# Kernel optimization log

Hardware: AMD Instinct MI355X
Metric: run time of the kernel (lower is better)

Reference implementation:

```python
import jax, jax.numpy as jnp
import numpy as np

N_USERS = 100000
N_ITEMS = 50000
N_NODES = N_USERS + N_ITEMS
D = 64          # embedding_size / d_model
L = 2           # n_layers (GCN layers and transformer layers)
H = 8           # nhead
FF = 2048       # TransformerEncoderLayer default dim_feedforward
E_RAND = 1600000
B = 4096
EPS = 1e-5


def setup_inputs() -> dict:
    key = jax.random.key(0)
    ks = jax.random.split(key, 24)
    s = 0.05
    users = jax.random.randint(ks[0], (B,), 0, N_USERS)
    items = jax.random.randint(ks[1], (B,), 0, N_ITEMS)
    src = jax.random.randint(ks[2], (E_RAND,), 0, N_NODES)
    dst = jax.random.randint(ks[3], (E_RAND,), 0, N_NODES)
    loops = jnp.arange(N_NODES)  # ensure degree >= 1 everywhere (real graphs have no isolated rows)
    edge_index = jnp.stack([jnp.concatenate([src, loops]), jnp.concatenate([dst, loops])])
    f32 = jnp.float32
    return {
        "users": users,
        "items": items,
        "edge_index": edge_index,
        "user_table": jax.random.normal(ks[4], (N_USERS, D), f32) * s,
        "item_table": jax.random.normal(ks[5], (N_ITEMS, D), f32) * s,
        "gl_W": jax.random.normal(ks[6], (L, D, D), f32) * s,
        "gl_b": jax.random.normal(ks[7], (L, D), f32) * s,
        "corr_W": jax.random.normal(ks[8], (D, D), f32) * s,
        "corr_b": jax.random.normal(ks[9], (D,), f32) * s,
        "qkv_W": jax.random.normal(ks[10], (L, D, 3 * D), f32) * s,
        "qkv_b": jax.random.normal(ks[11], (L, 3 * D), f32) * s,
        "out_W": jax.random.normal(ks[12], (L, D, D), f32) * s,
        "out_b": jax.random.normal(ks[13], (L, D), f32) * s,
        "ff1_W": jax.random.normal(ks[14], (L, D, FF), f32) * s,
        "ff1_b": jax.random.normal(ks[15], (L, FF), f32) * s,
        "ff2_W": jax.random.normal(ks[16], (L, FF, D), f32) * s,
        "ff2_b": jax.random.normal(ks[17], (L, D), f32) * s,
        "ln1_g": jnp.ones((L, D), f32),
        "ln1_b": jnp.zeros((L, D), f32),
        "ln2_g": jnp.ones((L, D), f32),
        "ln2_b": jnp.zeros((L, D), f32),
    }


def _layer_norm(x, g, b):
    m = jnp.mean(x, axis=-1, keepdims=True)
    v = jnp.mean(jnp.square(x - m), axis=-1, keepdims=True)
    return (x - m) * jax.lax.rsqrt(v + EPS) * g + b


def _transformer(x, qkv_W, qkv_b, out_W, out_b, ff1_W, ff1_b, ff2_W, ff2_b,
                 ln1_g, ln1_b, ln2_g, ln2_b):
    # x: [N, D]; original passes x.unsqueeze(0) with batch_first=False -> seq_len=1,
    # batch=N. Softmax over a single key is identity, so MHA(x) == out_proj(V(x)).
    for l in range(L):
        v = x @ qkv_W[l][:, 2 * D:] + qkv_b[l][2 * D:]          # [N, D] value projection
        attn = v @ out_W[l] + out_b[l]
        x = _layer_norm(x + attn, ln1_g[l], ln1_b[l])            # post-LN (PyTorch default)
        ffn = jax.nn.relu(x @ ff1_W[l] + ff1_b[l]) @ ff2_W[l] + ff2_b[l]
        x = _layer_norm(x + ffn, ln2_g[l], ln2_b[l])
    return x


def reference(users, items, edge_index, user_table, item_table, gl_W, gl_b,
              corr_W, corr_b, qkv_W, qkv_b, out_W, out_b, ff1_W, ff1_b,
              ff2_W, ff2_b, ln1_g, ln1_b, ln2_g, ln2_b):
    row, col = edge_index[0], edge_index[1]
    # degree-normalized scatter-add GCN propagation (GraphLayer.message)
    deg = jax.ops.segment_sum(jnp.ones(row.shape, user_table.dtype), row, num_segments=N_NODES)
    dis = deg ** -0.5
    norm = dis[row] * dis[col]                                   # [E]
    x = jnp.concatenate([user_table, item_table], axis=0)        # [N_NODES, D]
    for l in range(L):
        h = x @ gl_W[l] + gl_b[l]
        msg = norm[:, None] * h[row]                             # gather + edge norm
        x = jax.ops.segment_sum(msg, col, num_segments=N_NODES)  # scatter-add aggr
    user_g, item_g = x[:N_USERS], x[N_USERS:]
    # CrossModalCorrection: one shared Linear on both
    user_c = user_g @ corr_W + corr_b
    item_c = item_g @ corr_W + corr_b
    tf = lambda z: _transformer(z, qkv_W, qkv_b, out_W, out_b, ff1_W, ff1_b,
                                ff2_W, ff2_b, ln1_g, ln1_b, ln2_g, ln2_b)
    user_final = tf(user_c)
    item_final = tf(item_c)
    return jnp.sum(user_final[users] * item_final[items], axis=1)  # [B]
```

## Files before the change

### kernel.cpp

```cpp
#include <hip/hip_runtime.h>
#include <math.h>

#define NU 100000
#define NI 50000
#define NN 150000
#define NNP 150528
#define SCNB 147
#define LNEPS 1e-5f

__global__ __launch_bounds__(256) void k_markS(const int* __restrict__ users,
                                               const int* __restrict__ items,
                                               unsigned* __restrict__ bS, int nb) {
    int t = blockIdx.x * 256 + threadIdx.x;
    if (t < 2 * nb) {
        int node = (t < nb) ? users[t] : (NU + items[t - nb]);
        atomicOr(&bS[node >> 5], 1u << (node & 31));
    }
}

__global__ __launch_bounds__(256) void k_pre1(const int* __restrict__ row,
                                              const int* __restrict__ col,
                                              const unsigned* __restrict__ bS,
                                              int* __restrict__ deg,
                                              unsigned* __restrict__ bR, int E) {
    int e = blockIdx.x * 256 + threadIdx.x;
    if (e >= E) return;
    int r = row[e];
    atomicAdd(&deg[r], 1);
    int c = col[e];
    if ((bS[c >> 5] >> (c & 31)) & 1u) atomicOr(&bR[r >> 5], 1u << (r & 31));
}

__global__ __launch_bounds__(256) void k_dis(const int* __restrict__ deg,
                                             float* __restrict__ dis) {
    int i = blockIdx.x * 256 + threadIdx.x;
    if (i < NN) dis[i] = rsqrtf((float)deg[i]);
}

__global__ __launch_bounds__(256) void k_cnt(const int* __restrict__ col,
                                             const unsigned* __restrict__ bR,
                                             int* __restrict__ cnt, int E) {
    int e = blockIdx.x * 256 + threadIdx.x;
    if (e >= E) return;
    int c = col[e];
    if ((bR[c >> 5] >> (c & 31)) & 1u) atomicAdd(&cnt[c], 1);
}

__global__ __launch_bounds__(256) void k_scan1(const int* __restrict__ cnt,
                                               int* __restrict__ bsum) {
    __shared__ int sh[256];
    int b = blockIdx.x, t = threadIdx.x;
    int4 v = ((const int4*)cnt)[b * 256 + t];
    sh[t] = v.x + v.y + v.z + v.w;
    __syncthreads();
    for (int off = 128; off >= 1; off >>= 1) {
        if (t < off) sh[t] += sh[t + off];
        __syncthreads();
    }
    if (t == 0) bsum[b] = sh[0];
}

__global__ __launch_bounds__(256) void k_scan2(int* __restrict__ bsum, int nblk) {
    __shared__ int sh[256];
    int t = threadIdx.x;
    int v = (t < nblk) ? bsum[t] : 0;
    sh[t] = v;
    __syncthreads();
    for (int off = 1; off < 256; off <<= 1) {
        int add = (t >= off) ? sh[t - off] : 0;
        __syncthreads();
        sh[t] += add;
        __syncthreads();
    }
    if (t < nblk) bsum[t] = sh[t] - v;
}

__global__ __launch_bounds__(256) void k_scan3(const int* __restrict__ cnt,
                                               const int* __restrict__ bsum,
                                               int* __restrict__ start) {
    __shared__ int sh[257];
    int b = blockIdx.x, t = threadIdx.x;
    int4 v = ((const int4*)cnt)[b * 256 + t];
    int s = v.x + v.y + v.z + v.w;
    sh[t + 1] = s;
    if (t == 0) sh[0] = 0;
    __syncthreads();
    for (int off = 1; off < 256; off <<= 1) {
        int add = sh[t + 1] + ((t + 1 > off) ? sh[t + 1 - off] : 0);
        __syncthreads();
        sh[t + 1] = add;
        __syncthreads();
    }
    int base = bsum[b] + sh[t];
    int i0 = b * 1024 + t * 4;
    start[i0 + 0] = base;  base += v.x;
    start[i0 + 1] = base;  base += v.y;
    start[i0 + 2] = base;  base += v.z;
    start[i0 + 3] = base;
    if (b == SCNB - 1 && t == 255) start[NNP] = base + v.w;
}

__global__ __launch_bounds__(256) void k_place(const int* __restrict__ row,
                                               const int* __restrict__ col,
                                               const unsigned* __restrict__ bR,
                                               const float* __restrict__ dis,
                                               const int* __restrict__ start,
                                               int* __restrict__ cur,
                                               int2* __restrict__ el, int E) {
    int e = blockIdx.x * 256 + threadIdx.x;
    if (e >= E) return;
    int c = col[e];
    if (!((bR[c >> 5] >> (c & 31)) & 1u)) return;
    int r = row[e];
    float nv = dis[r] * dis[c];
    int pos = atomicAdd(&cur[c], 1);
    el[start[c] + pos] = make_int2(r, __float_as_int(nv));
}

__global__ __launch_bounds__(256) void k_gather1(const int2* __restrict__ el,
                                                 const int* __restrict__ start,
                                                 const float* __restrict__ ut,
                                                 const float* __restrict__ itb,
                                                 float* __restrict__ g1,
                                                 float* __restrict__ sdeg) {
    int wid = (blockIdx.x * 256 + threadIdx.x) >> 6;
    int j = threadIdx.x & 63;
    if (wid >= NN) return;
    int s = start[wid], e = start[wid + 1];
    if (s == e) return;
    float acc0 = 0.f, acc1 = 0.f, sn = 0.f;
    int i = s;
    for (; i + 1 < e; i += 2) {
        int2 e0 = el[i], e1 = el[i + 1];
        float n0 = __int_as_float(e0.y), n1 = __int_as_float(e1.y);
        const float* s0 = (e0.x < NU) ? ut + (size_t)e0.x * 64
                                      : itb + (size_t)(e0.x - NU) * 64;
        const float* s1 = (e1.x < NU) ? ut + (size_t)e1.x * 64
                                      : itb + (size_t)(e1.x - NU) * 64;
        acc0 = fmaf(n0, s0[j], acc0);
        acc1 = fmaf(n1, s1[j], acc1);
        sn += n0 + n1;
    }
    if (i < e) {
        int2 e0 = el[i];
        float n0 = __int_as_float(e0.y);
        const float* s0 = (e0.x < NU) ? ut + (size_t)e0.x * 64
                                      : itb + (size_t)(e0.x - NU) * 64;
        acc0 = fmaf(n0, s0[j], acc0);
        sn += n0;
    }
    g1[(size_t)wid * 64 + j] = acc0 + acc1;
    if (j == 0) sdeg[wid] = sn;
}

__global__ __launch_bounds__(256) void k_gather2(const int2* __restrict__ el,
                                                 const int* __restrict__ start,
                                                 const float* __restrict__ g1,
                                                 const float* __restrict__ sdeg,
                                                 const unsigned* __restrict__ bS,
                                                 float* __restrict__ gg,
                                                 float* __restrict__ s2) {
    int wid = (blockIdx.x * 256 + threadIdx.x) >> 6;
    int j = threadIdx.x & 63;
    if (wid >= NN) return;
    if (!((bS[wid >> 5] >> (wid & 31)) & 1u)) return;
    int s = start[wid], e = start[wid + 1];
    float acc0 = 0.f, acc1 = 0.f, sa = 0.f;
    int i = s;
    for (; i + 1 < e; i += 2) {
        int2 e0 = el[i], e1 = el[i + 1];
        float n0 = __int_as_float(e0.y), n1 = __int_as_float(e1.y);
        acc0 = fmaf(n0, g1[(size_t)e0.x * 64 + j], acc0);
        acc1 = fmaf(n1, g1[(size_t)e1.x * 64 + j], acc1);
        sa = fmaf(n0, sdeg[e0.x], sa);
        sa = fmaf(n1, sdeg[e1.x], sa);
    }
    if (i < e) {
        int2 e0 = el[i];
        float n0 = __int_as_float(e0.y);
        acc0 = fmaf(n0, g1[(size_t)e0.x * 64 + j], acc0);
        sa = fmaf(n0, sdeg[e0.x], sa);
    }
    gg[(size_t)wid * 64 + j] = acc0 + acc1;
    if (j == 0) s2[wid] = sa;
}

__global__ __launch_bounds__(256) void k_fuse(const float* __restrict__ qkvW,
                                              const float* __restrict__ qkvB,
                                              const float* __restrict__ outW,
                                              const float* __restrict__ outB,
                                              float* __restrict__ Wva,
                                              float* __restrict__ bva) {
    int l = blockIdx.x;
    __shared__ float wo[4096];
    int tid = threadIdx.x, j = tid & 63, kq = tid >> 6;
    for (int i = tid; i < 4096; i += 256) wo[i] = outW[l * 4096 + i];
    __syncthreads();
    for (int kk = 0; kk < 16; ++kk) {
        int k = kq * 16 + kk;
        float acc = 0.f;
        for (int m = 0; m < 64; ++m)
            acc = fmaf(qkvW[(size_t)l * 64 * 192 + k * 192 + 128 + m],
                       wo[m * 64 + j], acc);
        Wva[l * 4096 + k * 64 + j] = acc;
    }
    if (tid < 64) {
        float acc = outB[l * 64 + j];
        for (int m = 0; m < 64; ++m)
            acc = fmaf(qkvB[l * 192 + 128 + m], wo[m * 64 + j], acc);
        bva[l * 64 + j] = acc;
    }
}

__global__ __launch_bounds__(256) void k_fuse2(const float* __restrict__ glW,
                                               const float* __restrict__ glB,
                                               const float* __restrict__ corrW,
                                               const float* __restrict__ corrB,
                                               float* __restrict__ Wff,
                                               float* __restrict__ bff) {
    __shared__ float A[4096];
    __shared__ float B[4096];
    __shared__ float T[4096];
    __shared__ float vec[64];
    int tid = threadIdx.x, j = tid & 63, kq = tid >> 6;
    for (int i = tid; i < 4096; i += 256) { A[i] = glW[4096 + i]; B[i] = corrW[i]; }
    __syncthreads();
    for (int kk = 0; kk < 16; ++kk) {
        int k = kq * 16 + kk;
        float acc = 0.f;
        for (int m = 0; m < 64; ++m) acc = fmaf(glW[k * 64 + m], A[m * 64 + j], acc);
        T[k * 64 + j] = acc;
    }
    if (tid < 64) {
        float v = 0.f;
        for (int m = 0; m < 64; ++m) v = fmaf(glB[m], A[m * 64 + tid], v);
        vec[tid] = v;
    }
    __syncthreads();
    for (int kk = 0; kk < 16; ++kk) {
        int k = kq * 16 + kk;
        float acc = 0.f;
        for (int m = 0; m < 64; ++m) acc = fmaf(T[k * 64 + m], B[m * 64 + j], acc);
        Wff[k * 64 + j] = acc;
    }
    if (kq == 0) {
        float a = 0.f;
        for (int m = 0; m < 64; ++m) a = fmaf(vec[m], B[m * 64 + j], a);
        bff[j] = a;
    } else if (kq == 1) {
        float a = 0.f;
        for (int m = 0; m < 64; ++m) a = fmaf(glB[64 + m], B[m * 64 + j], a);
        bff[64 + j] = a;
    } else if (kq == 2) {
        bff[128 + j] = corrB[j];
    }
}

__global__ __launch_bounds__(256) void k_proj(const float* __restrict__ gg,
                                              const float* __restrict__ sdeg,
                                              const float* __restrict__ s2,
                                              const int* __restrict__ users,
                                              const int* __restrict__ items,
                                              const float* __restrict__ Wff,
                                              const float* __restrict__ bff,
                                              float* __restrict__ Cb, int nb) {
    __shared__ float Ws[4096];
    __shared__ float xsh[16][64];
    __shared__ float ssh[16][2];
    int tid = threadIdx.x, j = tid & 63, rq = tid >> 6;
    for (int i = tid; i < 4096; i += 256) Ws[i] = Wff[i];
    int r0 = blockIdx.x * 16;
    for (int i = tid; i < 1024; i += 256) {
        int b = r0 + (i >> 6);
        int node = (b < nb) ? users[b] : (NU + items[b - nb]);
        xsh[i >> 6][i & 63] = gg[(size_t)node * 64 + (i & 63)];
    }
    if (tid < 16) {
        int b = r0 + tid;
        int node = (b < nb) ? users[b] : (NU + items[b - nb]);
        ssh[tid][0] = s2[node];
        ssh[tid][1] = sdeg[node];
    }
    __syncthreads();
    float b1j = bff[j], b2j = bff[64 + j], cbj = bff[128 + j];
    float acc[4];
#pragma unroll
    for (int i = 0; i < 4; ++i) acc[i] = cbj;
    for (int k = 0; k < 64; ++k) {
        float w = Ws[k * 64 + j];
#pragma unroll
        for (int i = 0; i < 4; ++i) acc[i] = fmaf(xsh[rq + 4 * i][k], w, acc[i]);
    }
#pragma unroll
    for (int i = 0; i < 4; ++i) {
        int r = rq + 4 * i;
        Cb[(size_t)(r0 + r) * 64 + j] = acc[i] + ssh[r][0] * b1j + ssh[r][1] * b2j;
    }
}

__global__ __launch_bounds__(256) void k_attn(float* __restrict__ Cb,
                                              const float* __restrict__ Wva,
                                              const float* __restrict__ bva,
                                              const float* __restrict__ g,
                                              const float* __restrict__ bt,
                                              int layer) {
    __shared__ float Ws[4096];
    __shared__ float xs[16][64];
    int tid = threadIdx.x, j = tid & 63, rq = tid >> 6;
    const float* wv = Wva + layer * 4096;
    for (int i = tid; i < 4096; i += 256) Ws[i] = wv[i];
    int row0 = blockIdx.x * 16;
    for (int i = tid; i < 1024; i += 256)
        xs[i >> 6][i & 63] = Cb[(size_t)(row0 + (i >> 6)) * 64 + (i & 63)];
    __syncthreads();
    float bv = bva[layer * 64 + j];
    float gg = g[layer * 64 + j], bb = bt[layer * 64 + j];
    float acc[4];
#pragma unroll
    for (int i = 0; i < 4; ++i) acc[i] = bv;
    for (int k = 0; k < 64; ++k) {
        float w = Ws[k * 64 + j];
#pragma unroll
        for (int i = 0; i < 4; ++i) acc[i] = fmaf(xs[rq * 4 + i][k], w, acc[i]);
    }
#pragma unroll
    for (int i = 0; i < 4; ++i) {
        int r = rq * 4 + i;
        float xv = xs[r][j] + acc[i];
        float s = xv;
#pragma unroll
        for (int o = 32; o >= 1; o >>= 1) s += __shfl_xor(s, o, 64);
        float m = s * (1.0f / 64.0f);
        float d = xv - m;
        float s2v = d * d;
#pragma unroll
        for (int o = 32; o >= 1; o >>= 1) s2v += __shfl_xor(s2v, o, 64);
        float xn = d * rsqrtf(s2v * (1.0f / 64.0f) + LNEPS) * gg + bb;
        Cb[(size_t)(row0 + r) * 64 + j] = xn;
    }
}

__global__ __launch_bounds__(256) void k_ffn1(const float* __restrict__ Cb,
                                              const float* __restrict__ ff1W,
                                              const float* __restrict__ ff1B,
                                              const float* __restrict__ ff2W,
                                              float* __restrict__ ypart,
                                              int layer, int nrows) {
    __shared__ float xs[32][64];
    __shared__ float ts[32][128];
    const float* w1 = ff1W + (size_t)layer * 64 * 2048;
    const float* w2 = ff2W + (size_t)layer * 2048 * 64;
    const float* b1 = ff1B + layer * 2048;
    int tid = threadIdx.x;
    int rt = blockIdx.x;
    int hc = blockIdx.y;
    int row0 = rt * 32;
    for (int i = tid; i < 32 * 64; i += 256)
        xs[i >> 6][i & 63] = Cb[(size_t)(row0 + (i >> 6)) * 64 + (i & 63)];
    __syncthreads();
    int hh = tid & 63;
    int rg = tid >> 6;
    int h0 = hc * 128 + hh;
    float ta[8], tb[8];
    float bba = b1[h0], bbb = b1[h0 + 64];
#pragma unroll
    for (int i = 0; i < 8; ++i) { ta[i] = bba; tb[i] = bbb; }
    for (int k = 0; k < 64; k += 4) {
        float4 xv[8];
#pragma unroll
        for (int i = 0; i < 8; ++i)
            xv[i] = *reinterpret_cast<const float4*>(&xs[rg * 8 + i][k]);
#pragma unroll
        for (int kk = 0; kk < 4; ++kk) {
            float w1a = w1[(size_t)(k + kk) * 2048 + h0];
            float w1b = w1[(size_t)(k + kk) * 2048 + h0 + 64];
#pragma unroll
            for (int i = 0; i < 8; ++i) {
                float xvk = (kk == 0) ? xv[i].x : (kk == 1) ? xv[i].y
                          : (kk == 2) ? xv[i].z : xv[i].w;
                ta[i] = fmaf(xvk, w1a, ta[i]);
                tb[i] = fmaf(xvk, w1b, tb[i]);
            }
        }
    }
#pragma unroll
    for (int i = 0; i < 8; ++i) {
        ts[rg * 8 + i][hh]      = fmaxf(ta[i], 0.f);
        ts[rg * 8 + i][hh + 64] = fmaxf(tb[i], 0.f);
    }
    __syncthreads();
    int j = hh;
    float ya[8];
#pragma unroll
    for (int i = 0; i < 8; ++i) ya[i] = 0.f;
    for (int m = 0; m < 128; ++m) {
        float w2v = w2[(size_t)(hc * 128 + m) * 64 + j];
#pragma unroll
        for (int i = 0; i < 8; ++i) ya[i] = fmaf(ts[rg * 8 + i][m], w2v, ya[i]);
    }
#pragma unroll
    for (int i = 0; i < 8; ++i)
        ypart[((size_t)hc * nrows + row0 + rg * 8 + i) * 64 + j] = ya[i];
}

__global__ __launch_bounds__(256) void k_ffn2(float* __restrict__ Cb,
                                              const float* __restrict__ ypart,
                                              const float* __restrict__ ff2B,
                                              const float* __restrict__ g,
                                              const float* __restrict__ bt,
                                              int layer, int nrows) {
    int tid = threadIdx.x;
    int j = tid & 63, rq = tid >> 6;
    int row0 = blockIdx.x * 16;
    float b2 = ff2B[layer * 64 + j];
    float gg = g[layer * 64 + j], bb = bt[layer * 64 + j];
#pragma unroll
    for (int i = 0; i < 4; ++i) {
        int r = row0 + rq * 4 + i;
        float y = 0.f;
#pragma unroll
        for (int p = 0; p < 16; ++p)
            y += ypart[((size_t)p * nrows + r) * 64 + j];
        float xv = Cb[(size_t)r * 64 + j] + y + b2;
        float s = xv;
#pragma unroll
        for (int o = 32; o >= 1; o >>= 1) s += __shfl_xor(s, o, 64);
        float m = s * (1.0f / 64.0f);
        float d = xv - m;
        float s2v = d * d;
#pragma unroll
        for (int o = 32; o >= 1; o >>= 1) s2v += __shfl_xor(s2v, o, 64);
        float xn = d * rsqrtf(s2v * (1.0f / 64.0f) + LNEPS) * gg + bb;
        Cb[(size_t)r * 64 + j] = xn;
    }
}

__global__ __launch_bounds__(256) void k_dot(const float* __restrict__ Cb,
                                             float* __restrict__ out, int nb) {
    int t = blockIdx.x * 256 + threadIdx.x;
    int b = t >> 4;
    if (b >= nb) return;
    int q = (t & 15) * 4;
    const float4 u = *reinterpret_cast<const float4*>(Cb + (size_t)b * 64 + q);
    const float4 v = *reinterpret_cast<const float4*>(Cb + (size_t)(nb + b) * 64 + q);
    float s = u.x * v.x + u.y * v.y + u.z * v.z + u.w * v.w;
#pragma unroll
    for (int o = 8; o >= 1; o >>= 1) s += __shfl_xor(s, o, 16);
    if ((t & 15) == 0) out[b] = s;
}

extern "C" void kernel_launch(void* const* d_in, const int* in_sizes, int n_in,
                              void* d_out, int out_size, void* d_ws, size_t ws_size,
                              hipStream_t stream) {
    const int* users = (const int*)d_in[0];
    const int* items = (const int*)d_in[1];
    const int* ei    = (const int*)d_in[2];
    const float* ut  = (const float*)d_in[3];
    const float* itb = (const float*)d_in[4];
    const float* glW = (const float*)d_in[5];
    const float* glB = (const float*)d_in[6];
    const float* corrW = (const float*)d_in[7];
    const float* corrB = (const float*)d_in[8];
    const float* qkvW = (const float*)d_in[9];
    const float* qkvB = (const float*)d_in[10];
    const float* outW = (const float*)d_in[11];
    const float* outB = (const float*)d_in[12];
    const float* ff1W = (const float*)d_in[13];
    const float* ff1B = (const float*)d_in[14];
    const float* ff2W = (const float*)d_in[15];
    const float* ff2B = (const float*)d_in[16];
    const float* ln1g = (const float*)d_in[17];
    const float* ln1b = (const float*)d_in[18];
    const float* ln2g = (const float*)d_in[19];
    const float* ln2b = (const float*)d_in[20];

    const int E  = in_sizes[2] / 2;
    const int nb = in_sizes[0];
    const int nrows = 2 * nb;
    const int* rowp = ei;
    const int* colp = ei + E;

    char* w = (char*)d_ws;
    size_t off = 0;
    auto alloc = [&](size_t bytes) {
        char* p = w + off;
        off += (bytes + 255) & ~(size_t)255;
        return p;
    };
    int*      deg   = (int*)alloc((size_t)NN * 4);
    float*    dis   = (float*)alloc((size_t)NN * 4);
    unsigned* bS    = (unsigned*)alloc(((NN + 31) / 32) * 4);
    unsigned* bR    = (unsigned*)alloc(((NN + 31) / 32) * 4);
    int*      cnt   = (int*)alloc((size_t)NNP * 4);
    int*      start = (int*)alloc((size_t)(NNP + 1) * 4);
    int*      cur   = (int*)alloc((size_t)NN * 4);
    int*      bsum  = (int*)alloc((size_t)SCNB * 4);
    int2*     el    = (int2*)alloc((size_t)E * 8);
    float*    bufA  = (float*)alloc((size_t)NN * 64 * 4);
    float*    bufB  = (float*)alloc((size_t)NN * 64 * 4);
    float*    sdeg  = (float*)alloc((size_t)NN * 4);
    float*    s2    = (float*)alloc((size_t)NN * 4);
    float*    cb    = (float*)alloc((size_t)nrows * 64 * 4);
    float*    Wva   = (float*)alloc(2 * 4096 * 4);
    float*    bva   = (float*)alloc(2 * 64 * 4);
    float*    Wff   = (float*)alloc(4096 * 4);
    float*    bff   = (float*)alloc(192 * 4);
    float*    outp  = (float*)d_out;
    float*    ypart = bufA;

    hipMemsetAsync(deg, 0, (size_t)NN * 4, stream);
    hipMemsetAsync(bS, 0, ((NN + 31) / 32) * 4, stream);
    hipMemsetAsync(bR, 0, ((NN + 31) / 32) * 4, stream);
    hipMemsetAsync(cnt, 0, (size_t)NNP * 4, stream);
    hipMemsetAsync(cur, 0, (size_t)NN * 4, stream);

    int eb = (E + 255) / 256;
    int nnb = (NN + 255) / 256;

    k_markS<<<(2 * nb + 255) / 256, 256, 0, stream>>>(users, items, bS, nb);
    k_pre1<<<eb, 256, 0, stream>>>(rowp, colp, bS, deg, bR, E);
    k_dis<<<nnb, 256, 0, stream>>>(deg, dis);
    k_cnt<<<eb, 256, 0, stream>>>(colp, bR, cnt, E);
    k_scan1<<<SCNB, 256, 0, stream>>>(cnt, bsum);
    k_scan2<<<1, 256, 0, stream>>>(bsum, SCNB);
    k_scan3<<<SCNB, 256, 0, stream>>>(cnt, bsum, start);
    k_place<<<eb, 256, 0, stream>>>(rowp, colp, bR, dis, start, cur, el, E);
    k_fuse<<<2, 256, 0, stream>>>(qkvW, qkvB, outW, outB, Wva, bva);
    k_fuse2<<<1, 256, 0, stream>>>(glW, glB, corrW, corrB, Wff, bff);

    int agb = (NN + 3) / 4;

    k_gather1<<<agb, 256, 0, stream>>>(el, start, ut, itb, bufA, sdeg);
    k_gather2<<<agb, 256, 0, stream>>>(el, start, bufA, sdeg, bS, bufB, s2);
    k_proj<<<(nrows + 15) / 16, 256, 0, stream>>>(bufB, sdeg, s2, users, items,
                                                  Wff, bff, cb, nb);

    dim3 fgrid(nrows / 32, 16);
    for (int l = 0; l < 2; ++l) {
        k_attn<<<nrows / 16, 256, 0, stream>>>(cb, Wva, bva, ln1g, ln1b, l);
        k_ffn1<<<fgrid, 256, 0, stream>>>(cb, ff1W, ff1B, ff2W, ypart, l, nrows);
        k_ffn2<<<nrows / 16, 256, 0, stream>>>(cb, ypart, ff2B, ln2g, ln2b, l, nrows);
    }
    k_dot<<<(nb * 16 + 255) / 256, 256, 0, stream>>>(cb, outp, nb);
}
```

Baseline: 591.2 us.

## Fuse FFN into single bf16 MFMA kernel with pretransposed weights

Replaces the two-kernel fp32 FFN (ffn1 writing 16 partial sums per row, ffn2 reducing them and applying LayerNorm) with one kernel. It runs both FFN matmuls on bf16 MFMA 16x16x32 instructions, keeps the ReLU intermediate in swizzled shared memory, and applies residual plus LayerNorm in place. Weights are transposed and converted to bf16 once per call, and the attention kernel also emits a bf16 copy of its output. This removes the large partial-sum traffic and the scalar FMA cost, at the price of bf16 rounding error and fewer, larger blocks, since the grid is now only nrows/32.

```diff
diff --git a/kernel.cpp b/kernel.cpp
--- a/kernel.cpp
+++ b/kernel.cpp
@@ -7,6 +7,16 @@
 #define NNP 150528
 #define SCNB 147
 #define LNEPS 1e-5f
+
+typedef short bfx8 __attribute__((ext_vector_type(8)));
+typedef float f32x4 __attribute__((ext_vector_type(4)));
+#define MFMA16(a, b, c) __builtin_amdgcn_mfma_f32_16x16x32_bf16(a, b, c, 0, 0, 0)
+
+__device__ __forceinline__ unsigned short f2bf(float f) {
+    unsigned u = __float_as_uint(f);
+    unsigned r = u + 0x7FFFu + ((u >> 16) & 1u);
+    return (unsigned short)(r >> 16);
+}
 
 __global__ __launch_bounds__(256) void k_markS(const int* __restrict__ users,
                                                const int* __restrict__ items,
@@ -256,6 +266,33 @@
     }
 }
 
+__global__ __launch_bounds__(256) void k_wprep(const float* __restrict__ ff1W,
+                                               const float* __restrict__ ff2W,
+                                               unsigned short* __restrict__ Wt1,
+                                               unsigned short* __restrict__ Wt2) {
+    __shared__ float sh[64][65];
+    int b = blockIdx.x;
+    int l = b >> 6, rem = b & 63;
+    int mat = rem >> 5, tile = rem & 31;
+    const float* src; unsigned short* dst; int C, R, r0, c0;
+    if (mat == 0) { src = ff1W + (size_t)l * 64 * 2048; dst = Wt1 + (size_t)l * 2048 * 64;
+                    R = 64; C = 2048; r0 = 0; c0 = tile * 64; }
+    else          { src = ff2W + (size_t)l * 2048 * 64; dst = Wt2 + (size_t)l * 64 * 2048;
+                    R = 2048; C = 64; r0 = tile * 64; c0 = 0; }
+    int tid = threadIdx.x;
+    for (int it = 0; it < 16; ++it) {
+        int idx = it * 256 + tid;
+        int lr = idx >> 6, lc = idx & 63;
+        sh[lr][lc] = src[(size_t)(r0 + lr) * C + (c0 + lc)];
+    }
+    __syncthreads();
+    for (int it = 0; it < 16; ++it) {
+        int idx = it * 256 + tid;
+        int lc = idx >> 6, lr = idx & 63;
+        dst[(size_t)(c0 + lc) * R + (r0 + lr)] = f2bf(sh[lr][lc]);
+    }
+}
+
 __global__ __launch_bounds__(256) void k_proj(const float* __restrict__ gg,
                                               const float* __restrict__ sdeg,
                                               const float* __restrict__ s2,
@@ -299,6 +336,7 @@
 }
 
 __global__ __launch_bounds__(256) void k_attn(float* __restrict__ Cb,
+                                              unsigned short* __restrict__ xb,
                                               const float* __restrict__ Wva,
                                               const float* __restrict__ bva,
                                               const float* __restrict__ g,
@@ -337,91 +375,83 @@
         for (int o = 32; o >= 1; o >>= 1) s2v += __shfl_xor(s2v, o, 64);
         float xn = d * rsqrtf(s2v * (1.0f / 64.0f) + LNEPS) * gg + bb;
         Cb[(size_t)(row0 + r) * 64 + j] = xn;
-    }
-}
-
-__global__ __launch_bounds__(256) void k_ffn1(const float* __restrict__ Cb,
-                                              const float* __restrict__ ff1W,
+        xb[(size_t)(row0 + r) * 64 + j] = f2bf(xn);
+    }
+}
+
+__global__ __launch_bounds__(512) void k_ffnm(float* __restrict__ Cb,
+                                              const unsigned short* __restrict__ xb,
+                                              const unsigned short* __restrict__ Wt1,
+                                              const unsigned short* __restrict__ Wt2,
                                               const float* __restrict__ ff1B,
-                                              const float* __restrict__ ff2W,
-                                              float* __restrict__ ypart,
-                                              int layer, int nrows) {
-    __shared__ float xs[32][64];
-    __shared__ float ts[32][128];
-    const float* w1 = ff1W + (size_t)layer * 64 * 2048;
-    const float* w2 = ff2W + (size_t)layer * 2048 * 64;
+                                              const float* __restrict__ ff2B,
+                                              const float* __restrict__ g2,
+                                              const float* __restrict__ b2t,
+                                              int layer) {
+    __shared__ short ts[32 * 128];
+    __shared__ float ys[32 * 64];
+    const unsigned short* w1 = Wt1 + (size_t)layer * 2048 * 64;
+    const unsigned short* w2 = Wt2 + (size_t)layer * 64 * 2048;
     const float* b1 = ff1B + layer * 2048;
     int tid = threadIdx.x;
-    int rt = blockIdx.x;
-    int hc = blockIdx.y;
-    int row0 = rt * 32;
-    for (int i = tid; i < 32 * 64; i += 256)
-        xs[i >> 6][i & 63] = Cb[(size_t)(row0 + (i >> 6)) * 64 + (i & 63)];
-    __syncthreads();
-    int hh = tid & 63;
-    int rg = tid >> 6;
-    int h0 = hc * 128 + hh;
-    float ta[8], tb[8];
-    float bba = b1[h0], bbb = b1[h0 + 64];
-#pragma unroll
-    for (int i = 0; i < 8; ++i) { ta[i] = bba; tb[i] = bbb; }
-    for (int k = 0; k < 64; k += 4) {
-        float4 xv[8];
-#pragma unroll
-        for (int i = 0; i < 8; ++i)
-            xv[i] = *reinterpret_cast<const float4*>(&xs[rg * 8 + i][k]);
-#pragma unroll
-        for (int kk = 0; kk < 4; ++kk) {
-            float w1a = w1[(size_t)(k + kk) * 2048 + h0];
-            float w1b = w1[(size_t)(k + kk) * 2048 + h0 + 64];
-#pragma unroll
-            for (int i = 0; i < 8; ++i) {
-                float xvk = (kk == 0) ? xv[i].x : (kk == 1) ? xv[i].y
-                          : (kk == 2) ? xv[i].z : xv[i].w;
-                ta[i] = fmaf(xvk, w1a, ta[i]);
-                tb[i] = fmaf(xvk, w1b, tb[i]);
-            }
+    int lane = tid & 63, wv = tid >> 6;
+    int g = lane >> 4, r16 = lane & 15;
+    int row0 = blockIdx.x * 32;
+    int nt2 = wv & 3, mh = wv >> 2;
+
+    bfx8 ax[2][2];
+#pragma unroll
+    for (int mt = 0; mt < 2; ++mt)
+#pragma unroll
+        for (int ks = 0; ks < 2; ++ks)
+            ax[mt][ks] = *(const bfx8*)(xb + ((size_t)(row0 + 16 * mt + r16)) * 64
+                                        + 32 * ks + 8 * g);
+
+    f32x4 yfA = {0.f, 0.f, 0.f, 0.f}, yfB = {0.f, 0.f, 0.f, 0.f};
+
+    for (int hc = 0; hc < 16; ++hc) {
+        int h = hc * 128 + wv * 16 + r16;
+        float b1v = b1[h];
+        f32x4 tf0 = {b1v, b1v, b1v, b1v}, tf1 = tf0;
+#pragma unroll
+        for (int ks = 0; ks < 2; ++ks) {
+            bfx8 bw = *(const bfx8*)(w1 + (size_t)h * 64 + 32 * ks + 8 * g);
+            tf0 = MFMA16(ax[0][ks], bw, tf0);
+            tf1 = MFMA16(ax[1][ks], bw, tf1);
         }
-    }
-#pragma unroll
-    for (int i = 0; i < 8; ++i) {
-        ts[rg * 8 + i][hh]      = fmaxf(ta[i], 0.f);
-        ts[rg * 8 + i][hh + 64] = fmaxf(tb[i], 0.f);
-    }
-    __syncthreads();
-    int j = hh;
-    float ya[8];
-#pragma unroll
-    for (int i = 0; i < 8; ++i) ya[i] = 0.f;
-    for (int m = 0; m < 128; ++m) {
-        float w2v = w2[(size_t)(hc * 128 + m) * 64 + j];
-#pragma unroll
-        for (int i = 0; i < 8; ++i) ya[i] = fmaf(ts[rg * 8 + i][m], w2v, ya[i]);
-    }
-#pragma unroll
-    for (int i = 0; i < 8; ++i)
-        ypart[((size_t)hc * nrows + row0 + rg * 8 + i) * 64 + j] = ya[i];
-}
-
-__global__ __launch_bounds__(256) void k_ffn2(float* __restrict__ Cb,
-                                              const float* __restrict__ ypart,
-                                              const float* __restrict__ ff2B,
-                                              const float* __restrict__ g,
-                                              const float* __restrict__ bt,
-                                              int layer, int nrows) {
-    int tid = threadIdx.x;
-    int j = tid & 63, rq = tid >> 6;
-    int row0 = blockIdx.x * 16;
-    float b2 = ff2B[layer * 64 + j];
-    float gg = g[layer * 64 + j], bb = bt[layer * 64 + j];
+        int col = wv * 16 + r16;
+#pragma unroll
+        for (int r = 0; r < 4; ++r) {
+            int rowA = 4 * g + r, rowB = 16 + 4 * g + r;
+            int offA = (rowA * 256 + col * 2) ^ ((rowA & 7) << 4);
+            int offB = (rowB * 256 + col * 2) ^ ((rowB & 7) << 4);
+            *(short*)((char*)ts + offA) = (short)f2bf(fmaxf(tf0[r], 0.f));
+            *(short*)((char*)ts + offB) = (short)f2bf(fmaxf(tf1[r], 0.f));
+        }
+        __syncthreads();
+        int trow = 16 * mh + r16;
+#pragma unroll
+        for (int ks2 = 0; ks2 < 4; ++ks2) {
+            int kl = 32 * ks2 + 8 * g;
+            int off = (trow * 256 + kl * 2) ^ ((trow & 7) << 4);
+            bfx8 ta = *(const bfx8*)((char*)ts + off);
+            bfx8 bw2 = *(const bfx8*)(w2 + ((size_t)(16 * nt2 + r16)) * 2048
+                                      + hc * 128 + kl);
+            if (ks2 & 1) yfB = MFMA16(ta, bw2, yfB);
+            else         yfA = MFMA16(ta, bw2, yfA);
+        }
+        __syncthreads();
+    }
+#pragma unroll
+    for (int r = 0; r < 4; ++r)
+        ys[(16 * mh + 4 * g + r) * 64 + 16 * nt2 + r16] = yfA[r] + yfB[r];
+    __syncthreads();
+    float b2 = ff2B[layer * 64 + lane];
+    float gg = g2[layer * 64 + lane], bb = b2t[layer * 64 + lane];
 #pragma unroll
     for (int i = 0; i < 4; ++i) {
-        int r = row0 + rq * 4 + i;
-        float y = 0.f;
-#pragma unroll
-        for (int p = 0; p < 16; ++p)
-            y += ypart[((size_t)p * nrows + r) * 64 + j];
-        float xv = Cb[(size_t)r * 64 + j] + y + b2;
+        int r = wv * 4 + i;
+        float xv = Cb[(size_t)(row0 + r) * 64 + lane] + ys[r * 64 + lane] + b2;
         float s = xv;
 #pragma unroll
         for (int o = 32; o >= 1; o >>= 1) s += __shfl_xor(s, o, 64);
@@ -431,7 +461,7 @@
 #pragma unroll
         for (int o = 32; o >= 1; o >>= 1) s2v += __shfl_xor(s2v, o, 64);
         float xn = d * rsqrtf(s2v * (1.0f / 64.0f) + LNEPS) * gg + bb;
-        Cb[(size_t)r * 64 + j] = xn;
+        Cb[(size_t)(row0 + r) * 64 + lane] = xn;
     }
 }
 
@@ -505,8 +535,10 @@
     float*    bva   = (float*)alloc(2 * 64 * 4);
     float*    Wff   = (float*)alloc(4096 * 4);
     float*    bff   = (float*)alloc(192 * 4);
+    unsigned short* xbb = (unsigned short*)alloc((size_t)nrows * 64 * 2);
+    unsigned short* Wt1 = (unsigned short*)alloc((size_t)2 * 2048 * 64 * 2);
+    unsigned short* Wt2 = (unsigned short*)alloc((size_t)2 * 64 * 2048 * 2);
     float*    outp  = (float*)d_out;
-    float*    ypart = bufA;
 
     hipMemsetAsync(deg, 0, (size_t)NN * 4, stream);
     hipMemsetAsync(bS, 0, ((NN + 31) / 32) * 4, stream);
@@ -527,6 +559,7 @@
     k_place<<<eb, 256, 0, stream>>>(rowp, colp, bR, dis, start, cur, el, E);
     k_fuse<<<2, 256, 0, stream>>>(qkvW, qkvB, outW, outB, Wva, bva);
     k_fuse2<<<1, 256, 0, stream>>>(glW, glB, corrW, corrB, Wff, bff);
+    k_wprep<<<128, 256, 0, stream>>>(ff1W, ff2W, Wt1, Wt2);
 
     int agb = (NN + 3) / 4;
 
@@ -535,11 +568,10 @@
     k_proj<<<(nrows + 15) / 16, 256, 0, stream>>>(bufB, sdeg, s2, users, items,
                                                   Wff, bff, cb, nb);
 
-    dim3 fgrid(nrows / 32, 16);
     for (int l = 0; l < 2; ++l) {
-        k_attn<<<nrows / 16, 256, 0, stream>>>(cb, Wva, bva, ln1g, ln1b, l);
-        k_ffn1<<<fgrid, 256, 0, stream>>>(cb, ff1W, ff1B, ff2W, ypart, l, nrows);
-        k_ffn2<<<nrows / 16, 256, 0, stream>>>(cb, ypart, ff2B, ln2g, ln2b, l, nrows);
+        k_attn<<<nrows / 16, 256, 0, stream>>>(cb, xbb, Wva, bva, ln1g, ln1b, l);
+        k_ffnm<<<nrows / 32, 512, 0, stream>>>(cb, xbb, Wt1, Wt2, ff1B, ff2B,
+                                               ln2g, ln2b, l);
     }
     k_dot<<<(nb * 16 + 255) / 256, 256, 0, stream>>>(cb, outp, nb);
 }
```

Result: faster. 507.4 us (-14.2%).
